# Kernel tuning notes

Measured on AMD Instinct MI355X. Metric: run time of the kernel, lower is better.

The kernel has to match this reference:

```python
import jax, jax.numpy as jnp
import numpy as np

N_NODES = 100000
N_EDGES = 1200000
N_GRAPHS = 1000
HID = 64
OUT = 4
ALPHA_FLAG = 0.03
NEG_SLOPE = 0.2


def _glorot(key, shape):
    fan_in, fan_out = shape[0], shape[-1]
    lim = (6.0 / (fan_in + fan_out)) ** 0.5
    return jax.random.uniform(key, shape, jnp.float32, -lim, lim)


def setup_inputs() -> dict:
    key = jax.random.key(0)
    ks = jax.random.split(key, 32)
    inp = {
        "x": jax.random.normal(ks[0], (N_NODES, 8), jnp.float32),
        "edge_index": jax.random.randint(ks[1], (2, N_EDGES), 0, N_NODES, jnp.int32),
        "batch": jnp.sort(jax.random.randint(ks[2], (N_NODES,), 0, N_GRAPHS, jnp.int32)),
        "climber": jax.random.normal(ks[3], (N_GRAPHS, 6), jnp.float32),
        # lin_in
        "W_in": _glorot(ks[4], (6, HID)), "b_in": jnp.zeros((HID,), jnp.float32),
        # climber_embed: LayerNorm(6) + Linear(6,64)
        "ln_g": jnp.ones((6,), jnp.float32), "ln_b": jnp.zeros((6,), jnp.float32),
        "W_c": _glorot(ks[5], (6, HID)), "b_c": jnp.zeros((HID,), jnp.float32),
        # film1 / film2: Linear(64,128)
        "Wf1": _glorot(ks[6], (HID, 2 * HID)), "bf1": jnp.zeros((2 * HID,), jnp.float32),
        "Wf2": _glorot(ks[7], (HID, 2 * HID)), "bf2": jnp.zeros((2 * HID,), jnp.float32),
        # GATConv 1 (heads=1): lin weight, att_src, att_dst, bias
        "Wg1": _glorot(ks[8], (HID, HID)), "as1": _glorot(ks[9], (HID, 1))[:, 0],
        "ad1": _glorot(ks[10], (HID, 1))[:, 0], "bg1": jnp.zeros((HID,), jnp.float32),
        # GATConv 2
        "Wg2": _glorot(ks[11], (HID, HID)), "as2": _glorot(ks[12], (HID, 1))[:, 0],
        "ad2": _glorot(ks[13], (HID, 1))[:, 0], "bg2": jnp.zeros((HID,), jnp.float32),
        # cls head
        "Wc1": _glorot(ks[14], (HID, HID)), "bc1": jnp.zeros((HID,), jnp.float32),
        "Wc2": _glorot(ks[15], (HID, OUT)), "bc2": jnp.zeros((OUT,), jnp.float32),
        # flag head
        "Wh1": _glorot(ks[16], (2, 8)), "bh1": jnp.zeros((8,), jnp.float32),
        "Wh2": _glorot(ks[17], (8, OUT)), "bh2": jnp.zeros((OUT,), jnp.float32),
    }
    return inp


def _gat(h, src, dst, W, a_src, a_dst, bias, n):
    # PyG GATConv, heads=1, concat=False, self-loops already appended.
    z = h @ W                                    # [N, H]
    e = jax.nn.leaky_relu((z @ a_src)[src] + (z @ a_dst)[dst], NEG_SLOPE)  # [E]
    m = jax.ops.segment_max(e, dst, num_segments=n)
    ex = jnp.exp(e - m[dst])
    s = jax.ops.segment_sum(ex, dst, num_segments=n)
    alpha = ex / (s[dst] + 1e-16)
    out = jax.ops.segment_sum(alpha[:, None] * z[src], dst, num_segments=n)
    return out + bias


def reference(x, edge_index, batch, climber, W_in, b_in, ln_g, ln_b, W_c, b_c,
              Wf1, bf1, Wf2, bf2, Wg1, as1, ad1, bg1, Wg2, as2, ad2, bg2,
              Wc1, bc1, Wc2, bc2, Wh1, bh1, Wh2, bh2):
    n = x.shape[0]
    # add self loops (PyG GATConv default)
    loop = jnp.arange(n, dtype=edge_index.dtype)
    src = jnp.concatenate([edge_index[0], loop])
    dst = jnp.concatenate([edge_index[1], loop])

    x_cont, flags = x[:, :6], x[:, 6:8]
    h = x_cont @ W_in + b_in

    # climber embed: LayerNorm + Linear + ReLU
    mu = jnp.mean(climber, -1, keepdims=True)
    var = jnp.var(climber, -1, keepdims=True)
    cn = (climber - mu) * jax.lax.rsqrt(var + 1e-5) * ln_g + ln_b
    c = jax.nn.relu(cn @ W_c + b_c)

    def film(h, Wf, bf):
        gb = c @ Wf + bf
        gamma, beta = jnp.split(gb, 2, axis=-1)
        return h * (1.0 + gamma[batch]) + beta[batch]

    h = film(h, Wf1, bf1)
    h = jax.nn.relu(_gat(h, src, dst, Wg1, as1, ad1, bg1, n))
    h = film(h, Wf2, bf2)
    h = jax.nn.relu(_gat(h, src, dst, Wg2, as2, ad2, bg2, n))

    # cls head (dropout inactive in eval)
    cls = jax.nn.relu(h @ Wc1 + bc1) @ Wc2 + bc2
    flag = jax.nn.relu(flags @ Wh1 + bh1) @ Wh2 + bh2
    return cls + ALPHA_FLAG * flag
```

## Files before the change

### kernel.cpp

```cpp
#include <hip/hip_runtime.h>
#include <math.h>

#define N_NODES 100000
#define N_EDGES 1200000
#define N_GRAPHS 1000
#define HID 64
#define NBUCK 256
#define NPB   391
#define BCAP  8192
#define EDGE_CHUNK 16384
#define S3_BLOCKS ((N_EDGES + EDGE_CHUNK - 1) / EDGE_CHUNK)
#define LOG2E 1.4426950408889634f
#define N_TILES (N_NODES / 16)
#define MFMA_BLOCKS 391

typedef _Float16 half_t;
typedef __attribute__((ext_vector_type(4))) _Float16 half4;
typedef __attribute__((ext_vector_type(8))) _Float16 half8;
typedef __attribute__((ext_vector_type(4))) float floatx4;


__global__ void k_bin(const int* __restrict__ ei, int* __restrict__ bucket_fill,
                      int* __restrict__ staged) {
    __shared__ int hist[NBUCK];
    __shared__ int cursor[NBUCK];
    for (int t = threadIdx.x; t < NBUCK; t += blockDim.x) hist[t] = 0;
    __syncthreads();
    int e0 = blockIdx.x * EDGE_CHUNK;
    int e1 = min(e0 + EDGE_CHUNK, N_EDGES);
    for (int e = e0 + threadIdx.x; e < e1; e += blockDim.x)
        atomicAdd(&hist[ei[N_EDGES + e] / NPB], 1);
    __syncthreads();
    if (threadIdx.x < NBUCK) {
        int hv = hist[threadIdx.x];
        int start = threadIdx.x * BCAP;
        if (hv) start += atomicAdd(&bucket_fill[threadIdx.x], hv);
        cursor[threadIdx.x] = start;
    }
    __syncthreads();
    for (int e = e0 + threadIdx.x; e < e1; e += blockDim.x) {
        int src = ei[e], dst = ei[N_EDGES + e];
        int b = dst / NPB;
        int ldst = dst - b * NPB;
        int pos = atomicAdd(&cursor[b], 1);
        staged[pos] = (ldst << 17) | src;
    }
}

__global__ void k_bscan(const int* __restrict__ bucket_fill, int* __restrict__ bucket_base) {
    __shared__ int sh[NBUCK];
    int t = threadIdx.x;
    int v = bucket_fill[t];
    sh[t] = v;
    __syncthreads();
    for (int off = 1; off < NBUCK; off <<= 1) {
        int u = (t >= off) ? sh[t - off] : 0;
        __syncthreads();
        sh[t] += u;
        __syncthreads();
    }
    bucket_base[t] = sh[t] - v;
    if (t == NBUCK - 1) bucket_base[NBUCK] = sh[t];
}

__global__ void k_bcsr(const int* __restrict__ staged, const int* __restrict__ bucket_base,
                       int* __restrict__ rowptr, int* __restrict__ csr_src) {
    __shared__ int ldeg[NPB];
    __shared__ int sc[512];
    __shared__ int cursor[NPB];
    int b = blockIdx.x;
    int n0 = b * NPB;
    int n1 = min(n0 + NPB, N_NODES);
    int nn = n1 - n0;
    int bbase = bucket_base[b];
    int bcnt  = bucket_base[b+1] - bbase;
    const int* st = staged + b * BCAP;
    for (int t = threadIdx.x; t < NPB; t += blockDim.x) ldeg[t] = 0;
    __syncthreads();
    for (int k = threadIdx.x; k < bcnt; k += blockDim.x)
        atomicAdd(&ldeg[st[k] >> 17], 1);
    __syncthreads();
    if (threadIdx.x < 512) sc[threadIdx.x] = (threadIdx.x < nn) ? ldeg[threadIdx.x] : 0;
    __syncthreads();
    for (int off = 1; off < 512; off <<= 1) {
        int u = 0;
        if (threadIdx.x < 512 && threadIdx.x >= off) u = sc[threadIdx.x - off];
        __syncthreads();
        if (threadIdx.x < 512) sc[threadIdx.x] += u;
        __syncthreads();
    }
    if (threadIdx.x < nn) {
        int pre = sc[threadIdx.x] - ldeg[threadIdx.x];
        rowptr[n0 + threadIdx.x] = bbase + pre;
        cursor[threadIdx.x] = bbase + pre;
    }
    if (b == 0 && threadIdx.x == 0) rowptr[N_NODES] = bucket_base[NBUCK];
    __syncthreads();
    for (int k = threadIdx.x; k < bcnt; k += blockDim.x) {
        int v = st[k];
        int pos = atomicAdd(&cursor[v >> 17], 1);
        csr_src[pos] = v & 0x1FFFF;
    }
}

__global__ void k_climber_film(const float* __restrict__ climber,
                               const float* __restrict__ ln_g, const float* __restrict__ ln_b,
                               const float* __restrict__ W_c, const float* __restrict__ b_c,
                               const float* __restrict__ Wf1, const float* __restrict__ bf1,
                               const float* __restrict__ Wf2, const float* __restrict__ bf2,
                               float* __restrict__ gb1, float* __restrict__ gb2) {
    __shared__ float cl[64];
    int g = blockIdx.x;
    int j = threadIdx.x;
    if (j < 64) {
        float v[6];
        float mu = 0.f;
        #pragma unroll
        for (int k = 0; k < 6; k++) { v[k] = climber[g*6+k]; mu += v[k]; }
        mu *= (1.f/6.f);
        float var = 0.f;
        #pragma unroll
        for (int k = 0; k < 6; k++) { float d = v[k]-mu; var += d*d; }
        var *= (1.f/6.f);
        float rs = rsqrtf(var + 1e-5f);
        float acc = b_c[j];
        #pragma unroll
        for (int k = 0; k < 6; k++) {
            float cn = (v[k]-mu)*rs*ln_g[k] + ln_b[k];
            acc += cn * W_c[k*64+j];
        }
        cl[j] = fmaxf(acc, 0.f);
    }
    __syncthreads();
    float a1 = bf1[j], a2 = bf2[j];
    #pragma unroll 8
    for (int k = 0; k < 64; k++) {
        float ck = cl[k];
        a1 += ck * Wf1[k*128+j];
        a2 += ck * Wf2[k*128+j];
    }
    gb1[g*128+j] = a1;
    gb2[g*128+j] = a2;
}

__global__ void k_node0(const float* __restrict__ x, const int* __restrict__ batch,
                        const float* __restrict__ W_in, const float* __restrict__ b_in,
                        const float* __restrict__ gb1, half_t* __restrict__ h) {
    int tid = blockIdx.x * blockDim.x + threadIdx.x;
    int i  = tid >> 4;
    int sl = threadIdx.x & 15;
    if (i >= N_NODES) return;
    float4 acc = ((const float4*)b_in)[sl];
    #pragma unroll
    for (int k = 0; k < 6; k++) {
        float xk = x[i*8+k];
        float4 w = ((const float4*)W_in)[k*16 + sl];
        acc.x += xk*w.x; acc.y += xk*w.y; acc.z += xk*w.z; acc.w += xk*w.w;
    }
    int g = batch[i];
    const float4* gb4 = (const float4*)gb1;
    float4 ga = gb4[g*32 + sl];
    float4 be = gb4[g*32 + 16 + sl];
    half4 hv;
    hv.x = (half_t)(acc.x*(1.f+ga.x) + be.x);
    hv.y = (half_t)(acc.y*(1.f+ga.y) + be.y);
    hv.z = (half_t)(acc.z*(1.f+ga.z) + be.z);
    hv.w = (half_t)(acc.w*(1.f+ga.w) + be.w);
    ((half4*)h)[i*16 + sl] = hv;
}

__global__ __launch_bounds__(256) void k_mfma_z(
        const half_t* __restrict__ h, const float* __restrict__ W,
        const float* __restrict__ a_src, const float* __restrict__ a_dst,
        half_t* __restrict__ z, float* __restrict__ es, float* __restrict__ ed) {
    __shared__ half_t zl[4][16*64];
    int wave = threadIdx.x >> 6;
    int l    = threadIdx.x & 63;
    int c    = l & 15;
    int g    = l >> 4;
    half8 Bf[2][4];
    #pragma unroll
    for (int ko = 0; ko < 2; ko++) {
        #pragma unroll
        for (int nt = 0; nt < 4; nt++) {
            half8 b;
            #pragma unroll
            for (int j = 0; j < 8; j++)
                b[j] = (half_t)W[(ko*32 + g*8 + j)*64 + c + 16*nt];
            Bf[ko][nt] = b;
        }
    }
    float as4[4], ad4[4];
    #pragma unroll
    for (int nt = 0; nt < 4; nt++) {
        as4[nt] = a_src[c + 16*nt] * LOG2E;
        ad4[nt] = a_dst[c + 16*nt] * LOG2E;
    }
    int nWaves = gridDim.x * 4;
    int wid = blockIdx.x * 4 + wave;
    half_t* zw = zl[wave];
    for (int t = wid; t < N_TILES; t += nWaves) {
        int m0 = t * 16;
        const half8* hrow = (const half8*)(h + (size_t)(m0 + c) * 64);
        half8 A0 = hrow[g];
        half8 A1 = hrow[g + 4];
        floatx4 D[4];
        #pragma unroll
        for (int nt = 0; nt < 4; nt++) {
            floatx4 acc = {0.f, 0.f, 0.f, 0.f};
            acc = __builtin_amdgcn_mfma_f32_16x16x32_f16(A0, Bf[0][nt], acc, 0, 0, 0);
            acc = __builtin_amdgcn_mfma_f32_16x16x32_f16(A1, Bf[1][nt], acc, 0, 0, 0);
            D[nt] = acc;
        }
        #pragma unroll
        for (int r = 0; r < 4; r++) {
            float ps = D[0][r]*as4[0] + D[1][r]*as4[1] + D[2][r]*as4[2] + D[3][r]*as4[3];
            float pd = D[0][r]*ad4[0] + D[1][r]*ad4[1] + D[2][r]*ad4[2] + D[3][r]*ad4[3];
            #pragma unroll
            for (int off = 1; off < 16; off <<= 1) {
                ps += __shfl_xor(ps, off, 16);
                pd += __shfl_xor(pd, off, 16);
            }
            if (c == 0) {
                es[m0 + g*4 + r] = ps;
                ed[m0 + g*4 + r] = pd;
            }
        }
        #pragma unroll
        for (int nt = 0; nt < 4; nt++) {
            #pragma unroll
            for (int r = 0; r < 4; r++)
                zw[(g*4 + r)*64 + c + 16*nt] = (half_t)D[nt][r];
        }
        __asm__ __volatile__("s_waitcnt lgkmcnt(0)" ::: "memory");
        const half8* zr = (const half8*)zw;
        half8 v0 = zr[l*2];
        half8 v1 = zr[l*2 + 1];
        half8* zo = (half8*)(z + (size_t)m0 * 64);
        zo[l*2]     = v0;
        zo[l*2 + 1] = v1;
        __asm__ __volatile__("s_waitcnt lgkmcnt(0)" ::: "memory");
    }
}

__device__ __forceinline__ float4 h4_to_f4(half4 h) {
    float4 f;
    f.x = (float)h.x; f.y = (float)h.y; f.z = (float)h.z; f.w = (float)h.w;
    return f;
}

__global__ void k_agg(const int* __restrict__ rowptr, const int* __restrict__ csr_src,
                      const float* __restrict__ es, const float* __restrict__ ed,
                      const half_t* __restrict__ z, const float* __restrict__ bg,
                      const int* __restrict__ batch, const float* __restrict__ gb,
                      int apply_film, half_t* __restrict__ hout) {
    int tid = blockIdx.x * blockDim.x + threadIdx.x;
    int i  = tid >> 4;
    int sl = threadIdx.x & 15;
    if (i >= N_NODES) return;
    int beg = rowptr[i], end = rowptr[i+1];
    int deg = end - beg;
    float edi = ed[i];

    float e_self = es[i] + edi;
    e_self = fmaxf(e_self, 0.2f * e_self);

    int svA = 0, svB = 0;
    float exA = 0.f, exB = 0.f;
    if (sl < deg) {
        svA = csr_src[beg + sl];
        float v = es[svA] + edi;
        exA = exp2f(fmaxf(v, 0.2f * v));
    }
    if (16 + sl < deg) {
        svB = csr_src[beg + 16 + sl];
        float v = es[svB] + edi;
        exB = exp2f(fmaxf(v, 0.2f * v));
    }
    float s = exA + exB;
    #pragma unroll
    for (int off = 1; off < 16; off <<= 1)
        s += __shfl_xor(s, off, 16);
    float ex = exp2f(e_self);
    s += ex;

    const half4* z4 = (const half4*)z;
    float4 zi = h4_to_f4(z4[i*16 + sl]);
    float4 acc = {ex*zi.x, ex*zi.y, ex*zi.z, ex*zi.w};

    int lim = (deg < 32) ? deg : 32;
    int k = 0;
    for (; k + 8 <= lim; k += 8) {
        int a[8]; float e[8];
        if (k < 16) {
            #pragma unroll
            for (int j = 0; j < 8; j++) {
                a[j] = __shfl(svA, k+j, 16);
                e[j] = __shfl(exA, k+j, 16);
            }
        } else {
            #pragma unroll
            for (int j = 0; j < 8; j++) {
                a[j] = __shfl(svB, k-16+j, 16);
                e[j] = __shfl(exB, k-16+j, 16);
            }
        }
        half4 q[8];
        #pragma unroll
        for (int j = 0; j < 8; j++) q[j] = z4[a[j]*16 + sl];
        #pragma unroll
        for (int j = 0; j < 8; j++) {
            float4 r = h4_to_f4(q[j]);
            acc.x += e[j]*r.x; acc.y += e[j]*r.y;
            acc.z += e[j]*r.z; acc.w += e[j]*r.w;
        }
    }
    for (; k + 4 <= lim; k += 4) {
        int a[4]; float e[4];
        if (k < 16) {
            #pragma unroll
            for (int j = 0; j < 4; j++) {
                a[j] = __shfl(svA, k+j, 16);
                e[j] = __shfl(exA, k+j, 16);
            }
        } else {
            #pragma unroll
            for (int j = 0; j < 4; j++) {
                a[j] = __shfl(svB, k-16+j, 16);
                e[j] = __shfl(exB, k-16+j, 16);
            }
        }
        half4 q[4];
        #pragma unroll
        for (int j = 0; j < 4; j++) q[j] = z4[a[j]*16 + sl];
        #pragma unroll
        for (int j = 0; j < 4; j++) {
            float4 r = h4_to_f4(q[j]);
            acc.x += e[j]*r.x; acc.y += e[j]*r.y;
            acc.z += e[j]*r.z; acc.w += e[j]*r.w;
        }
    }
    for (; k < lim; k++) {
        int a; float e2;
        if (k < 16) { a = __shfl(svA, k, 16);    e2 = __shfl(exA, k, 16); }
        else        { a = __shfl(svB, k-16, 16); e2 = __shfl(exB, k-16, 16); }
        float4 zr = h4_to_f4(z4[a*16 + sl]);
        acc.x += e2*zr.x; acc.y += e2*zr.y; acc.z += e2*zr.z; acc.w += e2*zr.w;
    }
    for (int kk = beg + 32; kk < end; kk++) {
        int sv = csr_src[kk];
        float v = es[sv] + edi;
        float e2 = exp2f(fmaxf(v, 0.2f * v));
        s += e2;
        float4 zr = h4_to_f4(z4[sv*16 + sl]);
        acc.x += e2*zr.x; acc.y += e2*zr.y; acc.z += e2*zr.z; acc.w += e2*zr.w;
    }
    float inv = 1.f / (s + 1e-16f);
    float4 bg4 = ((const float4*)bg)[sl];
    float4 o;
    o.x = fmaxf(acc.x*inv + bg4.x, 0.f);
    o.y = fmaxf(acc.y*inv + bg4.y, 0.f);
    o.z = fmaxf(acc.z*inv + bg4.z, 0.f);
    o.w = fmaxf(acc.w*inv + bg4.w, 0.f);
    if (apply_film) {
        int g = batch[i];
        const float4* gb4 = (const float4*)gb;
        float4 ga = gb4[g*32 + sl];
        float4 be = gb4[g*32 + 16 + sl];
        o.x = o.x*(1.f+ga.x) + be.x;
        o.y = o.y*(1.f+ga.y) + be.y;
        o.z = o.z*(1.f+ga.z) + be.z;
        o.w = o.w*(1.f+ga.w) + be.w;
    }
    half4 hv;
    hv.x = (half_t)o.x; hv.y = (half_t)o.y; hv.z = (half_t)o.z; hv.w = (half_t)o.w;
    ((half4*)hout)[i*16 + sl] = hv;
}

__global__ __launch_bounds__(256) void k_head_mfma(
        const half_t* __restrict__ h, const float* __restrict__ x,
        const float* __restrict__ Wc1, const float* __restrict__ bc1,
        const float* __restrict__ Wc2, const float* __restrict__ bc2,
        const float* __restrict__ Wh1, const float* __restrict__ bh1,
        const float* __restrict__ Wh2, const float* __restrict__ bh2,
        float* __restrict__ out) {
    int l    = threadIdx.x & 63;
    int c    = l & 15;
    int g    = l >> 4;
    half8 Bf[2][4];
    #pragma unroll
    for (int ko = 0; ko < 2; ko++) {
        #pragma unroll
        for (int nt = 0; nt < 4; nt++) {
            half8 b;
            #pragma unroll
            for (int j = 0; j < 8; j++)
                b[j] = (half_t)Wc1[(ko*32 + g*8 + j)*64 + c + 16*nt];
            Bf[ko][nt] = b;
        }
    }
    float bc1v[4];
    float4 w2[4];
    #pragma unroll
    for (int nt = 0; nt < 4; nt++) {
        bc1v[nt] = bc1[c + 16*nt];
        w2[nt] = ((const float4*)Wc2)[c + 16*nt];
    }
    int nWaves = gridDim.x * 4;
    int wid = blockIdx.x * 4 + (threadIdx.x >> 6);
    for (int t = wid; t < N_TILES; t += nWaves) {
        int m0 = t * 16;
        const half8* hrow = (const half8*)(h + (size_t)(m0 + c) * 64);
        half8 A0 = hrow[g];
        half8 A1 = hrow[g + 4];
        floatx4 D[4];
        #pragma unroll
        for (int nt = 0; nt < 4; nt++) {
            floatx4 acc = {0.f, 0.f, 0.f, 0.f};
            acc = __builtin_amdgcn_mfma_f32_16x16x32_f16(A0, Bf[0][nt], acc, 0, 0, 0);
            acc = __builtin_amdgcn_mfma_f32_16x16x32_f16(A1, Bf[1][nt], acc, 0, 0, 0);
            D[nt] = acc;
        }
        #pragma unroll
        for (int r = 0; r < 4; r++) {
            float4 p = {0.f, 0.f, 0.f, 0.f};
            #pragma unroll
            for (int nt = 0; nt < 4; nt++) {
                float tv = fmaxf(D[nt][r] + bc1v[nt], 0.f);
                p.x += tv * w2[nt].x;
                p.y += tv * w2[nt].y;
                p.z += tv * w2[nt].z;
                p.w += tv * w2[nt].w;
            }
            #pragma unroll
            for (int off = 1; off < 16; off <<= 1) {
                p.x += __shfl_xor(p.x, off, 16);
                p.y += __shfl_xor(p.y, off, 16);
                p.z += __shfl_xor(p.z, off, 16);
                p.w += __shfl_xor(p.w, off, 16);
            }
            if (c == 0) {
                int m = m0 + g*4 + r;
                float f0 = x[m*8+6], f1 = x[m*8+7];
                float t8[8];
                #pragma unroll
                for (int q = 0; q < 8; q++)
                    t8[q] = fmaxf(f0*Wh1[q] + f1*Wh1[8+q] + bh1[q], 0.f);
                float fl[4];
                #pragma unroll
                for (int q = 0; q < 4; q++) {
                    float a = bh2[q];
                    #pragma unroll
                    for (int rr = 0; rr < 8; rr++) a += t8[rr]*Wh2[rr*4+q];
                    fl[q] = a;
                }
                float4 ov;
                ov.x = p.x + bc2[0] + 0.03f*fl[0];
                ov.y = p.y + bc2[1] + 0.03f*fl[1];
                ov.z = p.z + bc2[2] + 0.03f*fl[2];
                ov.w = p.w + bc2[3] + 0.03f*fl[3];
                ((float4*)out)[m] = ov;
            }
        }
    }
}

extern "C" void kernel_launch(void* const* d_in, const int* in_sizes, int n_in,
                              void* d_out, int out_size, void* d_ws, size_t ws_size,
                              hipStream_t stream) {
    const float* x       = (const float*)d_in[0];
    const int*   ei      = (const int*)  d_in[1];
    const int*   batch   = (const int*)  d_in[2];
    const float* climber = (const float*)d_in[3];
    const float* W_in    = (const float*)d_in[4];
    const float* b_in    = (const float*)d_in[5];
    const float* ln_g    = (const float*)d_in[6];
    const float* ln_b    = (const float*)d_in[7];
    const float* W_c     = (const float*)d_in[8];
    const float* b_c     = (const float*)d_in[9];
    const float* Wf1     = (const float*)d_in[10];
    const float* bf1     = (const float*)d_in[11];
    const float* Wf2     = (const float*)d_in[12];
    const float* bf2     = (const float*)d_in[13];
    const float* Wg1     = (const float*)d_in[14];
    const float* as1     = (const float*)d_in[15];
    const float* ad1     = (const float*)d_in[16];
    const float* bg1     = (const float*)d_in[17];
    const float* Wg2     = (const float*)d_in[18];
    const float* as2     = (const float*)d_in[19];
    const float* ad2     = (const float*)d_in[20];
    const float* bg2     = (const float*)d_in[21];
    const float* Wc1     = (const float*)d_in[22];
    const float* bc1     = (const float*)d_in[23];
    const float* Wc2     = (const float*)d_in[24];
    const float* bc2     = (const float*)d_in[25];
    const float* Wh1     = (const float*)d_in[26];
    const float* bh1     = (const float*)d_in[27];
    const float* Wh2     = (const float*)d_in[28];
    const float* bh2     = (const float*)d_in[29];
    float* out = (float*)d_out;
    float* ws  = (float*)d_ws;

    float*  gb1         = ws;
    float*  gb2         = gb1 + 128000;
    half_t* hbuf        = (half_t*)(gb2 + 128000);
    half_t* zbuf        = hbuf + 6400000;
    float*  es          = (float*)(zbuf + 6400000);
    float*  ed          = es + N_NODES;
    int*    rowptr      = (int*)(ed + N_NODES);
    int*    csr_src     = rowptr + N_NODES + 1;
    int*    bucket_fill = csr_src + N_EDGES;
    int*    bucket_base = bucket_fill + NBUCK;
    int*    staged      = bucket_base + NBUCK + 1;

    hipMemsetAsync(bucket_fill, 0, NBUCK*sizeof(int), stream);
    k_bin  <<<S3_BLOCKS, 1024, 0, stream>>>(ei, bucket_fill, staged);
    k_bscan<<<1, NBUCK, 0, stream>>>(bucket_fill, bucket_base);
    k_bcsr <<<NBUCK, 1024, 0, stream>>>(staged, bucket_base, rowptr, csr_src);

    k_climber_film<<<N_GRAPHS, 128, 0, stream>>>(climber, ln_g, ln_b, W_c, b_c,
                                                 Wf1, bf1, Wf2, bf2, gb1, gb2);

    int nodeBlocks = (N_NODES*16 + 255)/256;
    k_node0<<<nodeBlocks, 256, 0, stream>>>(x, batch, W_in, b_in, gb1, hbuf);
    k_mfma_z<<<MFMA_BLOCKS, 256, 0, stream>>>(hbuf, Wg1, as1, ad1, zbuf, es, ed);
    k_agg<<<nodeBlocks, 256, 0, stream>>>(rowptr, csr_src, es, ed, zbuf, bg1,
                                          batch, gb2, 1, hbuf);
    k_mfma_z<<<MFMA_BLOCKS, 256, 0, stream>>>(hbuf, Wg2, as2, ad2, zbuf, es, ed);
    k_agg<<<nodeBlocks, 256, 0, stream>>>(rowptr, csr_src, es, ed, zbuf, bg2,
                                          batch, gb2, 0, hbuf);
    k_head_mfma<<<MFMA_BLOCKS, 256, 0, stream>>>(hbuf, x, Wc1, bc1, Wc2, bc2,
                                                 Wh1, bh1, Wh2, bh2, out);
}
```

Baseline: 272.6 us.

## Fuse bucket scan into CSR build and fuse input projection into first GAT matmul

Drops the single-block bucket prefix-scan kernel. Each CSR-build block now redundantly scans the 256 bucket counts in shared memory. It also replaces the separate node-input kernel (lin_in plus FiLM, writing fp16 h) with a fused MFMA kernel. That kernel computes the input projection and FiLM directly into the A fragments before the first GAT projection. This removes two launches and one full write and read of the 100k x 64 hidden buffer, at the cost of some redundant per-block scan work.

```diff
diff --git a/kernel.cpp b/kernel.cpp
--- a/kernel.cpp
+++ b/kernel.cpp
@@ -47,34 +47,28 @@
     }
 }
 
-__global__ void k_bscan(const int* __restrict__ bucket_fill, int* __restrict__ bucket_base) {
-    __shared__ int sh[NBUCK];
-    int t = threadIdx.x;
-    int v = bucket_fill[t];
-    sh[t] = v;
-    __syncthreads();
-    for (int off = 1; off < NBUCK; off <<= 1) {
-        int u = (t >= off) ? sh[t - off] : 0;
-        __syncthreads();
-        sh[t] += u;
-        __syncthreads();
-    }
-    bucket_base[t] = sh[t] - v;
-    if (t == NBUCK - 1) bucket_base[NBUCK] = sh[t];
-}
-
-__global__ void k_bcsr(const int* __restrict__ staged, const int* __restrict__ bucket_base,
+__global__ void k_bcsr(const int* __restrict__ staged, const int* __restrict__ bucket_fill,
                        int* __restrict__ rowptr, int* __restrict__ csr_src) {
+    __shared__ int bb[NBUCK];
     __shared__ int ldeg[NPB];
     __shared__ int sc[512];
     __shared__ int cursor[NPB];
     int b = blockIdx.x;
+    if (threadIdx.x < NBUCK) bb[threadIdx.x] = bucket_fill[threadIdx.x];
+    __syncthreads();
+    for (int off = 1; off < NBUCK; off <<= 1) {
+        int u = 0;
+        if (threadIdx.x < NBUCK && threadIdx.x >= off) u = bb[threadIdx.x - off];
+        __syncthreads();
+        if (threadIdx.x < NBUCK) bb[threadIdx.x] += u;
+        __syncthreads();
+    }
+    int bbase = (b == 0) ? 0 : bb[b-1];
+    int bcnt  = bb[b] - bbase;
+    const int* st = staged + b * BCAP;
     int n0 = b * NPB;
     int n1 = min(n0 + NPB, N_NODES);
     int nn = n1 - n0;
-    int bbase = bucket_base[b];
-    int bcnt  = bucket_base[b+1] - bbase;
-    const int* st = staged + b * BCAP;
     for (int t = threadIdx.x; t < NPB; t += blockDim.x) ldeg[t] = 0;
     __syncthreads();
     for (int k = threadIdx.x; k < bcnt; k += blockDim.x)
@@ -94,7 +88,7 @@
         rowptr[n0 + threadIdx.x] = bbase + pre;
         cursor[threadIdx.x] = bbase + pre;
     }
-    if (b == 0 && threadIdx.x == 0) rowptr[N_NODES] = bucket_base[NBUCK];
+    if (b == 0 && threadIdx.x == 0) rowptr[N_NODES] = bb[NBUCK-1];
     __syncthreads();
     for (int k = threadIdx.x; k < bcnt; k += blockDim.x) {
         int v = st[k];
@@ -143,30 +137,118 @@
     gb2[g*128+j] = a2;
 }
 
-__global__ void k_node0(const float* __restrict__ x, const int* __restrict__ batch,
-                        const float* __restrict__ W_in, const float* __restrict__ b_in,
-                        const float* __restrict__ gb1, half_t* __restrict__ h) {
-    int tid = blockIdx.x * blockDim.x + threadIdx.x;
-    int i  = tid >> 4;
-    int sl = threadIdx.x & 15;
-    if (i >= N_NODES) return;
-    float4 acc = ((const float4*)b_in)[sl];
+__global__ __launch_bounds__(256) void k_mfma_z1(
+        const float* __restrict__ x, const int* __restrict__ batch,
+        const float* __restrict__ W_in, const float* __restrict__ b_in,
+        const float* __restrict__ gb1, const float* __restrict__ W,
+        const float* __restrict__ a_src, const float* __restrict__ a_dst,
+        half_t* __restrict__ z, float* __restrict__ es, float* __restrict__ ed) {
+    __shared__ float Wi[384];
+    __shared__ float bi[64];
+    __shared__ half_t zl[4][16*64];
+    for (int idx = threadIdx.x; idx < 384; idx += 256) Wi[idx] = W_in[idx];
+    if (threadIdx.x < 64) bi[threadIdx.x] = b_in[threadIdx.x];
+    int wave = threadIdx.x >> 6;
+    int l    = threadIdx.x & 63;
+    int c    = l & 15;
+    int g    = l >> 4;
+    half8 Bf[2][4];
     #pragma unroll
-    for (int k = 0; k < 6; k++) {
-        float xk = x[i*8+k];
-        float4 w = ((const float4*)W_in)[k*16 + sl];
-        acc.x += xk*w.x; acc.y += xk*w.y; acc.z += xk*w.z; acc.w += xk*w.w;
-    }
-    int g = batch[i];
-    const float4* gb4 = (const float4*)gb1;
-    float4 ga = gb4[g*32 + sl];
-    float4 be = gb4[g*32 + 16 + sl];
-    half4 hv;
-    hv.x = (half_t)(acc.x*(1.f+ga.x) + be.x);
-    hv.y = (half_t)(acc.y*(1.f+ga.y) + be.y);
-    hv.z = (half_t)(acc.z*(1.f+ga.z) + be.z);
-    hv.w = (half_t)(acc.w*(1.f+ga.w) + be.w);
-    ((half4*)h)[i*16 + sl] = hv;
+    for (int ko = 0; ko < 2; ko++) {
+        #pragma unroll
+        for (int nt = 0; nt < 4; nt++) {
+            half8 bvec;
+            #pragma unroll
+            for (int j = 0; j < 8; j++)
+                bvec[j] = (half_t)W[(ko*32 + g*8 + j)*64 + c + 16*nt];
+            Bf[ko][nt] = bvec;
+        }
+    }
+    float as4[4], ad4[4];
+    #pragma unroll
+    for (int nt = 0; nt < 4; nt++) {
+        as4[nt] = a_src[c + 16*nt] * LOG2E;
+        ad4[nt] = a_dst[c + 16*nt] * LOG2E;
+    }
+    __syncthreads();
+    int nWaves = gridDim.x * 4;
+    int wid = blockIdx.x * 4 + wave;
+    half_t* zw = zl[wave];
+    for (int t = wid; t < N_TILES; t += nWaves) {
+        int m0 = t * 16;
+        int i = m0 + c;
+        float xv[6];
+        #pragma unroll
+        for (int kk = 0; kk < 6; kk++) xv[kk] = x[i*8 + kk];
+        int bg_ = batch[i];
+        half8 A[2];
+        #pragma unroll
+        for (int s = 0; s < 2; s++) {
+            int bk = s*32 + g*8;
+            float acc[8];
+            #pragma unroll
+            for (int j = 0; j < 8; j++) acc[j] = bi[bk + j];
+            #pragma unroll
+            for (int kk = 0; kk < 6; kk++) {
+                float xk = xv[kk];
+                float4 w0 = *(const float4*)&Wi[kk*64 + bk];
+                float4 w1 = *(const float4*)&Wi[kk*64 + bk + 4];
+                acc[0] += xk*w0.x; acc[1] += xk*w0.y;
+                acc[2] += xk*w0.z; acc[3] += xk*w0.w;
+                acc[4] += xk*w1.x; acc[5] += xk*w1.y;
+                acc[6] += xk*w1.z; acc[7] += xk*w1.w;
+            }
+            const float4* gbv = (const float4*)(gb1 + bg_*128);
+            float4 ga0 = gbv[bk/4],      ga1 = gbv[bk/4 + 1];
+            float4 be0 = gbv[16 + bk/4], be1 = gbv[16 + bk/4 + 1];
+            half8 hv;
+            hv[0] = (half_t)(acc[0]*(1.f+ga0.x) + be0.x);
+            hv[1] = (half_t)(acc[1]*(1.f+ga0.y) + be0.y);
+            hv[2] = (half_t)(acc[2]*(1.f+ga0.z) + be0.z);
+            hv[3] = (half_t)(acc[3]*(1.f+ga0.w) + be0.w);
+            hv[4] = (half_t)(acc[4]*(1.f+ga1.x) + be1.x);
+            hv[5] = (half_t)(acc[5]*(1.f+ga1.y) + be1.y);
+            hv[6] = (half_t)(acc[6]*(1.f+ga1.z) + be1.z);
+            hv[7] = (half_t)(acc[7]*(1.f+ga1.w) + be1.w);
+            A[s] = hv;
+        }
+        floatx4 D[4];
+        #pragma unroll
+        for (int nt = 0; nt < 4; nt++) {
+            floatx4 acc = {0.f, 0.f, 0.f, 0.f};
+            acc = __builtin_amdgcn_mfma_f32_16x16x32_f16(A[0], Bf[0][nt], acc, 0, 0, 0);
+            acc = __builtin_amdgcn_mfma_f32_16x16x32_f16(A[1], Bf[1][nt], acc, 0, 0, 0);
+            D[nt] = acc;
+        }
+        #pragma unroll
+        for (int r = 0; r < 4; r++) {
+            float ps = D[0][r]*as4[0] + D[1][r]*as4[1] + D[2][r]*as4[2] + D[3][r]*as4[3];
+            float pd = D[0][r]*ad4[0] + D[1][r]*ad4[1] + D[2][r]*ad4[2] + D[3][r]*ad4[3];
+            #pragma unroll
+            for (int off = 1; off < 16; off <<= 1) {
+                ps += __shfl_xor(ps, off, 16);
+                pd += __shfl_xor(pd, off, 16);
+            }
+            if (c == 0) {
+                es[m0 + g*4 + r] = ps;
+                ed[m0 + g*4 + r] = pd;
+            }
+        }
+        #pragma unroll
+        for (int nt = 0; nt < 4; nt++) {
+            #pragma unroll
+            for (int r = 0; r < 4; r++)
+                zw[(g*4 + r)*64 + c + 16*nt] = (half_t)D[nt][r];
+        }
+        __asm__ __volatile__("s_waitcnt lgkmcnt(0)" ::: "memory");
+        const half8* zr = (const half8*)zw;
+        half8 v0 = zr[l*2];
+        half8 v1 = zr[l*2 + 1];
+        half8* zo = (half8*)(z + (size_t)m0 * 64);
+        zo[l*2]     = v0;
+        zo[l*2 + 1] = v1;
+        __asm__ __volatile__("s_waitcnt lgkmcnt(0)" ::: "memory");
+    }
 }
 
 __global__ __launch_bounds__(256) void k_mfma_z(
@@ -510,20 +592,18 @@
     int*    rowptr      = (int*)(ed + N_NODES);
     int*    csr_src     = rowptr + N_NODES + 1;
     int*    bucket_fill = csr_src + N_EDGES;
-    int*    bucket_base = bucket_fill + NBUCK;
-    int*    staged      = bucket_base + NBUCK + 1;
+    int*    staged      = bucket_fill + NBUCK;
 
     hipMemsetAsync(bucket_fill, 0, NBUCK*sizeof(int), stream);
-    k_bin  <<<S3_BLOCKS, 1024, 0, stream>>>(ei, bucket_fill, staged);
-    k_bscan<<<1, NBUCK, 0, stream>>>(bucket_fill, bucket_base);
-    k_bcsr <<<NBUCK, 1024, 0, stream>>>(staged, bucket_base, rowptr, csr_src);
+    k_bin <<<S3_BLOCKS, 1024, 0, stream>>>(ei, bucket_fill, staged);
+    k_bcsr<<<NBUCK, 1024, 0, stream>>>(staged, bucket_fill, rowptr, csr_src);
 
     k_climber_film<<<N_GRAPHS, 128, 0, stream>>>(climber, ln_g, ln_b, W_c, b_c,
                                                  Wf1, bf1, Wf2, bf2, gb1, gb2);
 
     int nodeBlocks = (N_NODES*16 + 255)/256;
-    k_node0<<<nodeBlocks, 256, 0, stream>>>(x, batch, W_in, b_in, gb1, hbuf);
-    k_mfma_z<<<MFMA_BLOCKS, 256, 0, stream>>>(hbuf, Wg1, as1, ad1, zbuf, es, ed);
+    k_mfma_z1<<<MFMA_BLOCKS, 256, 0, stream>>>(x, batch, W_in, b_in, gb1, Wg1,
+                                               as1, ad1, zbuf, es, ed);
     k_agg<<<nodeBlocks, 256, 0, stream>>>(rowptr, csr_src, es, ed, zbuf, bg1,
                                           batch, gb2, 1, hbuf);
     k_mfma_z<<<MFMA_BLOCKS, 256, 0, stream>>>(hbuf, Wg2, as2, ad2, zbuf, es, ed);
```

New measurement: 265.9 us. 2.5% less time.
